# Performance work log

Hardware: AMD Instinct MI355X
Metric: run time of the kernel (lower is better)

## Reference

```python
import jax, jax.numpy as jnp
import numpy as np

N, CIN, PL, H, W, ETA, EXP = 8, 1024, 256, 64, 64, 8, 4
EPS = 1e-5

def _conv(x, w, stride=1, pad=0):
    return jax.lax.conv_general_dilated(
        x, w, (stride, stride), [(pad, pad), (pad, pad)],
        dimension_numbers=('NCHW', 'OIHW', 'NCHW'))

def _bn(x, p):
    # p: [4, C] = gamma, beta, running_mean, running_var (eval-mode BN)
    g, b, m, v = p[0], p[1], p[2], p[3]
    scale = (g / jnp.sqrt(v + EPS))[None, :, None, None]
    return (x - m[None, :, None, None]) * scale + b[None, :, None, None]

def _bn_params(key, c):
    k1, k2, k3, k4 = jax.random.split(key, 4)
    return jnp.stack([
        1.0 + 0.1 * jax.random.normal(k1, (c,)),
        0.1 * jax.random.normal(k2, (c,)),
        0.1 * jax.random.normal(k3, (c,)),
        jax.random.uniform(k4, (c,), minval=0.5, maxval=1.5)]).astype(jnp.float32)

def setup_inputs() -> dict:
    key = jax.random.key(0)
    ks = jax.random.split(key, 12)
    return {
        'x': jax.random.normal(ks[0], (N, CIN, H, W), jnp.float32),
        'norm_1': jnp.zeros((1, N + 1), jnp.float32),
        'norm_2': jnp.zeros((1, N + 1), jnp.float32),
        'flops': jnp.zeros((1, N + 1), jnp.float32),
        'ws_conv': 0.02 * jax.random.normal(ks[1], (1, CIN, 3, 3), jnp.float32),
        'ws_bias': jnp.zeros((1,), jnp.float32),
        'wc1': 0.02 * jax.random.normal(ks[2], (PL, CIN), jnp.float32),
        'bc1': jnp.zeros((PL,), jnp.float32),
        'wc2': 0.02 * jax.random.normal(ks[3], (PL, PL), jnp.float32),
        'bc2': jnp.zeros((PL,), jnp.float32),
        'w1': 0.05 * jax.random.normal(ks[4], (PL, CIN, 1, 1), jnp.float32),
        'bn1': _bn_params(ks[5], PL),
        'w2': 0.02 * jax.random.normal(ks[6], (PL, PL, 3, 3), jnp.float32),
        'bn2': _bn_params(ks[7], PL),
        'w3': 0.05 * jax.random.normal(ks[8], (PL * EXP, PL, 1, 1), jnp.float32),
        'bn3': _bn_params(ks[9], PL * EXP),
    }

def reference(x, norm_1, norm_2, flops, ws_conv, ws_bias, wc1, bc1, wc2, bc2,
              w1, bn1, w2, bn2, w3, bn3):
    n, c, h1, w1s = x.shape
    dt = x.dtype
    # ---- Mask_s: avg-pool by eta -> 3x3 conv to 1 ch -> hard gate (eval) ----
    pooled = x.reshape(n, c, h1 // ETA, ETA, w1s // ETA, ETA).mean((3, 5))
    logit_s = _conv(pooled, ws_conv, pad=1) + ws_bias[None, :, None, None]
    mask_s_m = (logit_s >= 0).astype(dt)            # [n,1,h/eta,w/eta]
    norm_s = mask_s_m.sum((1, 2, 3))                # [n]
    # ---- Mask_c1: GAP -> FC -> hard gate -> [n,PL,1,1] ----
    vec1 = x.mean((2, 3))                            # [n,CIN]
    mc1 = ((vec1 @ wc1.T + bc1) >= 0).astype(dt)[:, :, None, None]
    norm_c1 = mc1.sum((1, 2, 3))
    norm_c1_t = jnp.array([PL], dt)
    # ---- main path ----
    out = jax.nn.relu(_bn(_conv(x, w1), bn1))
    # nearest upsample of spatial mask back to (h1, w1)
    mask_s1 = jnp.repeat(jnp.repeat(mask_s_m, ETA, axis=2), ETA, axis=3)
    out = out * mc1 * mask_s1                        # eval-mode: both masks applied
    # ---- Mask_c2 on gated features ----
    vec2 = out.mean((2, 3))
    mc2 = ((vec2 @ wc2.T + bc2) >= 0).astype(dt)[:, :, None, None]
    norm_c2 = mc2.sum((1, 2, 3))
    norm_c2_t = jnp.array([PL], dt)
    out = jax.nn.relu(_bn(_conv(out, w2, pad=1), bn2))
    h2, w2s = out.shape[2], out.shape[3]
    mask_s2 = mask_s1                                # stride=1 -> same spatial size
    out = out * mc2 * mask_s2
    out = _bn(_conv(out, w3), bn3) * mask_s2
    out = jax.nn.relu(out + x)                       # identity (downsample=None)
    # ---- bookkeeping ----
    numel_s = jnp.array([mask_s_m[0].size], dt)      # 1 * h/eta * w/eta
    norm_1 = jnp.concatenate([norm_1, jnp.concatenate([norm_s, numel_s])[None]], 0)
    norm_2 = jnp.concatenate([norm_2, jnp.concatenate([norm_c1, norm_c1_t])[None]], 0)
    norm_2 = jnp.concatenate([norm_2, jnp.concatenate([norm_c2, norm_c2_t])[None]], 0)
    s_sum = mask_s2.sum((1, 2, 3))
    s_sum_1 = mask_s1.sum((1, 2, 3))
    fl = (s_sum_1 * norm_c1 * CIN
          + 9.0 * s_sum * norm_c2 * norm_c1
          + s_sum * (PL * EXP) * norm_c2)
    fl_full = jnp.array([h1 * w1s * PL * CIN
                         + 9 * h2 * w2s * PL * PL
                         + h2 * w2s * PL * PL * EXP], dt)
    flops = jnp.concatenate([flops, jnp.concatenate([fl, fl_full])[None]], 0)
    return out, norm_1, norm_2, flops
```

## Files before the change

kernel.cpp:

```cpp
#include <hip/hip_runtime.h>
#include <cstddef>
#include <cstdint>

#define NN   8
#define CIN  1024
#define PL   256
#define PE   1024
#define HW   4096
#define EPS_ 1e-5f

typedef _Float16 half8 __attribute__((ext_vector_type(8)));
typedef float floatx4 __attribute__((ext_vector_type(4)));

union HU { uint4 u4; half8 h8; };

__device__ inline uint32_t pack2(float v) {
  union { _Float16 f[2]; uint32_t u; } z;
  _Float16 h = (_Float16)v;
  z.f[0] = h;
  z.f[1] = (_Float16)(v - (float)h);
  return z.u;
}

static const size_t OFF1 = 33554432;
static const size_t OFF2 = OFF1 + 18;
static const size_t OFF3 = OFF2 + 27;

__global__ __launch_bounds__(256) void k_prep(
    const float* __restrict__ bn1, const float* __restrict__ bn2,
    const float* __restrict__ bn3, const float* __restrict__ w1,
    const float* __restrict__ w2, const float* __restrict__ w3,
    _Float16* __restrict__ w1h, _Float16* __restrict__ w1l,
    _Float16* __restrict__ w2h, _Float16* __restrict__ w2l,
    _Float16* __restrict__ w3h, _Float16* __restrict__ w3l,
    float* __restrict__ s1, float* __restrict__ t1,
    float* __restrict__ s2, float* __restrict__ t2,
    float* __restrict__ s3, float* __restrict__ t3,
    float* __restrict__ vec2) {
  int idx = blockIdx.x * 256 + threadIdx.x;
  if (idx < 262144) {
    float v = w1[idx]; _Float16 h = (_Float16)v;
    w1h[idx] = h; w1l[idx] = (_Float16)(v - (float)h);
  } else if (idx < 524288) {
    int i = idx - 262144;
    float v = w3[i]; _Float16 h = (_Float16)v;
    w3h[i] = h; w3l[i] = (_Float16)(v - (float)h);
  } else if (idx < 1114112) {
    int i = idx - 524288;
    int tap = i >> 16, rem = i & 65535, p = rem >> 8, c = rem & 255;
    float v = w2[((p << 8) + c) * 9 + tap];
    _Float16 h = (_Float16)v;
    w2h[i] = h; w2l[i] = (_Float16)(v - (float)h);
  } else if (idx < 1116160) {
    vec2[idx - 1114112] = 0.f;
  } else if (idx < 1117696) {
    int i = idx - 1116160;
    if (i < 256) {
      float g = bn1[i], b = bn1[256 + i], m = bn1[512 + i], v = bn1[768 + i];
      float s = g / sqrtf(v + EPS_);
      s1[i] = s; t1[i] = b - m * s;
    } else if (i < 512) {
      int c = i - 256;
      float g = bn2[c], b = bn2[256 + c], m = bn2[512 + c], v = bn2[768 + c];
      float s = g / sqrtf(v + EPS_);
      s2[c] = s; t2[c] = b - m * s;
    } else {
      int c = i - 512;
      float g = bn3[c], b = bn3[1024 + c], m = bn3[2048 + c], v = bn3[3072 + c];
      float s = g / sqrtf(v + EPS_);
      s3[c] = s; t3[c] = b - m * s;
    }
  }
}

__global__ __launch_bounds__(64) void k_pool(const float* __restrict__ x,
                                             float* __restrict__ pooled,
                                             float* __restrict__ vec1) {
  const int bx = blockIdx.x;
  const int n = bx >> 10, c = bx & 1023;
  const int t = threadIdx.x;
  const float* xp = x + (size_t)(n * CIN + c) * HW;
  const int g = t >> 3;
  float v1 = 0.f;
  for (int ph = 0; ph < 8; ++ph) {
    float a = 0.f;
#pragma unroll
    for (int r = 0; r < 8; ++r) a += xp[(ph * 8 + r) * 64 + t];
    a += __shfl_xor(a, 1, 64);
    a += __shfl_xor(a, 2, 64);
    a += __shfl_xor(a, 4, 64);
    if ((t & 7) == 0)
      pooled[(size_t)(n * 64 + ph * 8 + g) * 1024 + c] = a * (1.f / 64.f);
    v1 += a;
  }
  v1 += __shfl_xor(v1, 8, 64);
  v1 += __shfl_xor(v1, 16, 64);
  v1 += __shfl_xor(v1, 32, 64);
  if (t == 0) vec1[n * 1024 + c] = v1 * (1.f / 4096.f);
}

__global__ __launch_bounds__(256) void k_masks(const float* __restrict__ wsconv,
                                               const float* __restrict__ wsbias,
                                               const float* __restrict__ pooled,
                                               float* __restrict__ masks) {
  const int bid = blockIdx.x;
  const int n = bid >> 6, cell = bid & 63, ph = cell >> 3, pw = cell & 7;
  const int tid = threadIdx.x;
  const float* pl = pooled + (size_t)n * 64 * 1024;
  float acc = 0.f;
#pragma unroll
  for (int kh = 0; kh < 3; ++kh) {
    int py = ph + kh - 1;
    if (py < 0 || py > 7) continue;
#pragma unroll
    for (int kw = 0; kw < 3; ++kw) {
      int px = pw + kw - 1;
      if (px < 0 || px > 7) continue;
      float4 pv = *(const float4*)(pl + (size_t)(py * 8 + px) * 1024 + tid * 4);
      int k = kh * 3 + kw;
      acc += pv.x * wsconv[(tid * 4 + 0) * 9 + k] + pv.y * wsconv[(tid * 4 + 1) * 9 + k]
           + pv.z * wsconv[(tid * 4 + 2) * 9 + k] + pv.w * wsconv[(tid * 4 + 3) * 9 + k];
    }
  }
  __shared__ float red[256];
  red[tid] = acc;
  __syncthreads();
  for (int s = 128; s > 0; s >>= 1) {
    if (tid < s) red[tid] += red[tid + s];
    __syncthreads();
  }
  if (tid == 0) masks[n * 64 + cell] = (red[0] + wsbias[0] >= 0.f) ? 1.f : 0.f;
}

__global__ __launch_bounds__(64) void k_mc1(const float* __restrict__ wc1,
                                            const float* __restrict__ bc1,
                                            const float* __restrict__ vec1,
                                            float* __restrict__ mc1) {
  const int bx = blockIdx.x;
  const int n = bx >> 8, p = bx & 255;
  const int t = threadIdx.x;
  const float* v = vec1 + n * 1024;
  const float* wr = wc1 + (size_t)p * 1024;
  float acc = 0.f;
#pragma unroll
  for (int j = 0; j < 16; ++j) acc += v[t + 64 * j] * wr[t + 64 * j];
  for (int m = 1; m < 64; m <<= 1) acc += __shfl_xor(acc, m, 64);
  if (t == 0) mc1[n * 256 + p] = (acc + bc1[p] >= 0.f) ? 1.f : 0.f;
}

__global__ __launch_bounds__(256) void k_xsplit(const float* __restrict__ x,
                                                _Float16* __restrict__ xh,
                                                _Float16* __restrict__ xl) {
  const int hw0 = blockIdx.x * 64, c0 = blockIdx.y * 64, n = blockIdx.z;
  const int t = threadIdx.x;
  __shared__ float Tt[64][65];
#pragma unroll
  for (int j = 0; j < 4; ++j) {
    int rc = (t >> 4) + j * 16;
    int col = (t & 15) * 4;
    float4 v = *(const float4*)(x + ((size_t)(n * 1024) + c0 + rc) * 4096 + hw0 + col);
    Tt[col + 0][rc] = v.x; Tt[col + 1][rc] = v.y;
    Tt[col + 2][rc] = v.z; Tt[col + 3][rc] = v.w;
  }
  __syncthreads();
  const int hwl = t >> 2, part = t & 3;
  size_t ob = ((size_t)(n * 4096) + hw0 + hwl) * 1024 + c0 + part * 16;
#pragma unroll
  for (int k2 = 0; k2 < 2; ++k2) {
    half8 vh, vl;
#pragma unroll
    for (int e = 0; e < 8; ++e) {
      float v = Tt[hwl][part * 16 + k2 * 8 + e];
      _Float16 hh = (_Float16)v;
      vh[e] = hh; vl[e] = (_Float16)(v - (float)hh);
    }
    *(half8*)(xh + ob + k2 * 8) = vh;
    *(half8*)(xl + ob + k2 * 8) = vl;
  }
}

__global__ __launch_bounds__(256) void k_gemm1(
    const _Float16* __restrict__ xh, const _Float16* __restrict__ xl,
    const _Float16* __restrict__ w1h, const _Float16* __restrict__ w1l,
    const float* __restrict__ s1, const float* __restrict__ t1,
    const float* __restrict__ mc1, const float* __restrict__ masks,
    _Float16* __restrict__ o1h, _Float16* __restrict__ o1l) {
  const int hw0 = blockIdx.x * 128, p0 = blockIdx.y * 128, n = blockIdx.z;
  const int t = threadIdx.x;
  const int lane = t & 63, w = t >> 6;
  const int l15 = lane & 15, l4 = lane >> 4;
  const int wr = w >> 1, wc = w & 1;
  __shared__ __align__(16) char smem[40960];
  _Float16* LB = (_Float16*)smem;
  floatx4 acc[4][4] = {};
  const size_t nb = (size_t)(n * 4096) + hw0;
  for (int ks = 0; ks < 32; ++ks) {
    const int c0 = ks * 32;
    half8 tmp[8];
#pragma unroll
    for (int j = 0; j < 8; ++j) {
      int u = t + 256 * j;
      int kind = u >> 9, rem = u & 511, row = rem >> 2, q = rem & 3;
      const _Float16* src;
      if (kind == 0)      src = w1h + (size_t)(p0 + row) * 1024 + c0 + q * 8;
      else if (kind == 1) src = w1l + (size_t)(p0 + row) * 1024 + c0 + q * 8;
      else if (kind == 2) src = xh + (nb + row) * 1024 + c0 + q * 8;
      else                src = xl + (nb + row) * 1024 + c0 + q * 8;
      tmp[j] = *(const half8*)src;
    }
    __syncthreads();
#pragma unroll
    for (int j = 0; j < 8; ++j) {
      int u = t + 256 * j;
      int kind = u >> 9, rem = u & 511, row = rem >> 2, q = rem & 3;
      *(half8*)(LB + kind * 5120 + row * 40 + q * 8) = tmp[j];
    }
    __syncthreads();
    half8 ah[4], al[4], bh[4], bl[4];
#pragma unroll
    for (int i = 0; i < 4; ++i) {
      int r = (wr * 64 + i * 16 + l15) * 40 + l4 * 8;
      ah[i] = *(const half8*)(LB + r);
      al[i] = *(const half8*)(LB + 5120 + r);
    }
#pragma unroll
    for (int j = 0; j < 4; ++j) {
      int r = (wc * 64 + j * 16 + l15) * 40 + l4 * 8;
      bh[j] = *(const half8*)(LB + 10240 + r);
      bl[j] = *(const half8*)(LB + 15360 + r);
    }
#pragma unroll
    for (int i = 0; i < 4; ++i)
#pragma unroll
      for (int j = 0; j < 4; ++j) {
        acc[i][j] = __builtin_amdgcn_mfma_f32_16x16x32_f16(ah[i], bh[j], acc[i][j], 0, 0, 0);
        acc[i][j] = __builtin_amdgcn_mfma_f32_16x16x32_f16(ah[i], bl[j], acc[i][j], 0, 0, 0);
        acc[i][j] = __builtin_amdgcn_mfma_f32_16x16x32_f16(al[i], bh[j], acc[i][j], 0, 0, 0);
      }
  }
  uint32_t (*T)[132] = (uint32_t(*)[132])smem;
  const int n64 = n * 64;
  const float* mc1n = mc1 + n * 256;
  for (int h = 0; h < 2; ++h) {
    __syncthreads();
    if (wc == h) {
#pragma unroll
      for (int j = 0; j < 4; ++j) {
        int nl = j * 16 + l15;
        int pix = hw0 + h * 64 + nl;
        float msk = masks[n64 + ((pix >> 9) << 3) + ((pix & 63) >> 3)];
#pragma unroll
        for (int i = 0; i < 4; ++i) {
          uint32_t pk[4];
#pragma unroll
          for (int r = 0; r < 4; ++r) {
            int m = wr * 64 + i * 16 + l4 * 4 + r;
            int p = p0 + m;
            float val = fmaxf(fmaf(acc[i][j][r], s1[p], t1[p]), 0.f) * (mc1n[p] * msk);
            pk[r] = pack2(val);
          }
          *(uint4*)&T[nl][wr * 64 + i * 16 + l4 * 4] = *(uint4*)pk;
        }
      }
    }
    __syncthreads();
    {
      int row = t >> 2, seg = t & 3;
      int pix = hw0 + h * 64 + row;
      _Float16* dh = o1h + ((size_t)(n * 4096) + pix) * 256 + p0 + seg * 32;
      _Float16* dl = o1l + ((size_t)(n * 4096) + pix) * 256 + p0 + seg * 32;
#pragma unroll
      for (int k2 = 0; k2 < 4; ++k2) {
        uint4 a = *(uint4*)&T[row][seg * 32 + k2 * 8];
        uint4 b = *(uint4*)&T[row][seg * 32 + k2 * 8 + 4];
        uint4 hv = make_uint4((a.x & 0xFFFFu) | (a.y << 16), (a.z & 0xFFFFu) | (a.w << 16),
                              (b.x & 0xFFFFu) | (b.y << 16), (b.z & 0xFFFFu) | (b.w << 16));
        uint4 lv = make_uint4((a.x >> 16) | (a.y & 0xFFFF0000u), (a.z >> 16) | (a.w & 0xFFFF0000u),
                              (b.x >> 16) | (b.y & 0xFFFF0000u), (b.z >> 16) | (b.w & 0xFFFF0000u));
        *(uint4*)(dh + k2 * 8) = hv;
        *(uint4*)(dl + k2 * 8) = lv;
      }
    }
  }
}

__global__ __launch_bounds__(256) void k_vec2(const _Float16* __restrict__ o1h,
                                              const _Float16* __restrict__ o1l,
                                              float* __restrict__ vec2) {
  const int n = blockIdx.x >> 5, ch = blockIdx.x & 31;
  const int t = threadIdx.x;
  const _Float16* bh = o1h + ((size_t)(n * 4096) + ch * 128) * 256 + t;
  const _Float16* bl = o1l + ((size_t)(n * 4096) + ch * 128) * 256 + t;
  float s = 0.f;
  for (int i = 0; i < 128; ++i)
    s += (float)bh[(size_t)i * 256] + (float)bl[(size_t)i * 256];
  atomicAdd(&vec2[n * 256 + t], s * (1.f / 4096.f));
}

__global__ __launch_bounds__(64) void k_mc2(const float* __restrict__ wc2,
                                            const float* __restrict__ bc2,
                                            const float* __restrict__ vec2,
                                            float* __restrict__ mc2) {
  const int bx = blockIdx.x;
  const int n = bx >> 8, p = bx & 255;
  const int t = threadIdx.x;
  const float* v = vec2 + n * 256;
  const float* wr = wc2 + (size_t)p * 256;
  float acc = 0.f;
#pragma unroll
  for (int j = 0; j < 4; ++j) acc += v[t + 64 * j] * wr[t + 64 * j];
  for (int m = 1; m < 64; m <<= 1) acc += __shfl_xor(acc, m, 64);
  if (t == 0) mc2[n * 256 + p] = (acc + bc2[p] >= 0.f) ? 1.f : 0.f;
}

__global__ __launch_bounds__(256) void k_gemm2(
    const _Float16* __restrict__ o1h, const _Float16* __restrict__ o1l,
    const _Float16* __restrict__ w2h, const _Float16* __restrict__ w2l,
    const float* __restrict__ s2, const float* __restrict__ t2,
    const float* __restrict__ mc2, const float* __restrict__ masks,
    _Float16* __restrict__ o2h, _Float16* __restrict__ o2l) {
  const int bt = blockIdx.x, p0 = blockIdx.y * 128, n = blockIdx.z;
  const int hw0 = bt * 128;
  const int t = threadIdx.x;
  const int lane = t & 63, w = t >> 6;
  const int l15 = lane & 15, l4 = lane >> 4;
  const int wr = w >> 1, wc = w & 1;
  __shared__ __align__(16) char smem[62720];
  _Float16* LB = (_Float16*)smem;
  floatx4 acc[4][4] = {};
  const size_t onb = (size_t)(n * 4096);
  const int row0 = bt * 2 - 1;
  for (int c0 = 0; c0 < 256; c0 += 32) {
    HU st[9];
#pragma unroll
    for (int j2 = 0; j2 < 9; ++j2) {
      int u = t + 256 * j2;
      st[j2].u4 = make_uint4(0u, 0u, 0u, 0u);
      if (u < 2112) {
        int kind = (u >= 1056) ? 1 : 0;
        int rem = u - kind * 1056;
        int pix = rem >> 2, q = rem & 3;
        int sr = pix / 66, sc = pix - sr * 66;
        int gr = row0 + sr, gc = sc - 1;
        if (gr >= 0 && gr < 64 && gc >= 0 && gc < 64) {
          const _Float16* src = (kind ? o1l : o1h) + (onb + gr * 64 + gc) * 256 + c0 + q * 8;
          st[j2].h8 = *(const half8*)src;
        }
      }
    }
    __syncthreads();
#pragma unroll
    for (int j2 = 0; j2 < 9; ++j2) {
      int u = t + 256 * j2;
      if (u < 2112) {
        int kind = (u >= 1056) ? 1 : 0;
        int rem = u - kind * 1056;
        int pix = rem >> 2, q = rem & 3;
        *(half8*)(LB + kind * 10560 + pix * 40 + q * 8) = st[j2].h8;
      }
    }
    for (int tap = 0; tap < 9; ++tap) {
      const int kh = tap / 3, kw = tap - kh * 3;
      HU at[4];
#pragma unroll
      for (int j2 = 0; j2 < 4; ++j2) {
        int u = t + 256 * j2;
        int kind = u >> 9, rem = u & 511, row = rem >> 2, q = rem & 3;
        const _Float16* src = (kind ? w2l : w2h) + (size_t)tap * 65536 +
                              (size_t)(p0 + row) * 256 + c0 + q * 8;
        at[j2].h8 = *(const half8*)src;
      }
      __syncthreads();
#pragma unroll
      for (int j2 = 0; j2 < 4; ++j2) {
        int u = t + 256 * j2;
        int kind = u >> 9, rem = u & 511, row = rem >> 2, q = rem & 3;
        *(half8*)(LB + 21120 + kind * 5120 + row * 40 + q * 8) = at[j2].h8;
      }
      __syncthreads();
      half8 ah[4], al[4], bh[4], bl[4];
#pragma unroll
      for (int i = 0; i < 4; ++i) {
        int r = (wr * 64 + i * 16 + l15) * 40 + l4 * 8;
        ah[i] = *(const half8*)(LB + 21120 + r);
        al[i] = *(const half8*)(LB + 26240 + r);
      }
#pragma unroll
      for (int j = 0; j < 4; ++j) {
        int nl = wc * 64 + j * 16 + l15;
        int pi = ((nl >> 6) + kh) * 66 + (nl & 63) + kw;
        bh[j] = *(const half8*)(LB + pi * 40 + l4 * 8);
        bl[j] = *(const half8*)(LB + 10560 + pi * 40 + l4 * 8);
      }
#pragma unroll
      for (int i = 0; i < 4; ++i)
#pragma unroll
        for (int j = 0; j < 4; ++j) {
          acc[i][j] = __builtin_amdgcn_mfma_f32_16x16x32_f16(ah[i], bh[j], acc[i][j], 0, 0, 0);
          acc[i][j] = __builtin_amdgcn_mfma_f32_16x16x32_f16(ah[i], bl[j], acc[i][j], 0, 0, 0);
          acc[i][j] = __builtin_amdgcn_mfma_f32_16x16x32_f16(al[i], bh[j], acc[i][j], 0, 0, 0);
        }
    }
    __syncthreads();
  }
  uint32_t (*T)[132] = (uint32_t(*)[132])smem;
  const int n64 = n * 64;
  const float* mc2n = mc2 + n * 256;
  for (int h = 0; h < 2; ++h) {
    __syncthreads();
    if (wc == h) {
#pragma unroll
      for (int j = 0; j < 4; ++j) {
        int nl = j * 16 + l15;
        int pix = hw0 + h * 64 + nl;
        float msk = masks[n64 + ((pix >> 9) << 3) + ((pix & 63) >> 3)];
#pragma unroll
        for (int i = 0; i < 4; ++i) {
          uint32_t pk[4];
#pragma unroll
          for (int r = 0; r < 4; ++r) {
            int m = wr * 64 + i * 16 + l4 * 4 + r;
            int p = p0 + m;
            float val = fmaxf(fmaf(acc[i][j][r], s2[p], t2[p]), 0.f) * (mc2n[p] * msk);
            pk[r] = pack2(val);
          }
          *(uint4*)&T[nl][wr * 64 + i * 16 + l4 * 4] = *(uint4*)pk;
        }
      }
    }
    __syncthreads();
    {
      int row = t >> 2, seg = t & 3;
      int pix = hw0 + h * 64 + row;
      _Float16* dh = o2h + ((size_t)(n * 4096) + pix) * 256 + p0 + seg * 32;
      _Float16* dl = o2l + ((size_t)(n * 4096) + pix) * 256 + p0 + seg * 32;
#pragma unroll
      for (int k2 = 0; k2 < 4; ++k2) {
        uint4 a = *(uint4*)&T[row][seg * 32 + k2 * 8];
        uint4 b = *(uint4*)&T[row][seg * 32 + k2 * 8 + 4];
        uint4 hv = make_uint4((a.x & 0xFFFFu) | (a.y << 16), (a.z & 0xFFFFu) | (a.w << 16),
                              (b.x & 0xFFFFu) | (b.y << 16), (b.z & 0xFFFFu) | (b.w << 16));
        uint4 lv = make_uint4((a.x >> 16) | (a.y & 0xFFFF0000u), (a.z >> 16) | (a.w & 0xFFFF0000u),
                              (b.x >> 16) | (b.y & 0xFFFF0000u), (b.z >> 16) | (b.w & 0xFFFF0000u));
        *(uint4*)(dh + k2 * 8) = hv;
        *(uint4*)(dl + k2 * 8) = lv;
      }
    }
  }
}

__global__ __launch_bounds__(256) void k_gemm3(
    const _Float16* __restrict__ o2h, const _Float16* __restrict__ o2l,
    const _Float16* __restrict__ w3h, const _Float16* __restrict__ w3l,
    const float* __restrict__ s3, const float* __restrict__ t3,
    const float* __restrict__ masks, const float* __restrict__ x,
    float* __restrict__ out) {
  const int hw0 = blockIdx.x * 128, p0 = blockIdx.y * 128, n = blockIdx.z;
  const int t = threadIdx.x;
  const int lane = t & 63, w = t >> 6;
  const int l15 = lane & 15, l4 = lane >> 4;
  const int wr = w >> 1, wc = w & 1;
  __shared__ __align__(16) char smem[40960];
  _Float16* LB = (_Float16*)smem;
  floatx4 acc[4][4] = {};
  const size_t nb = (size_t)(n * 4096) + hw0;
  for (int ks = 0; ks < 8; ++ks) {
    const int c0 = ks * 32;
    half8 tmp[8];
#pragma unroll
    for (int j = 0; j < 8; ++j) {
      int u = t + 256 * j;
      int kind = u >> 9, rem = u & 511, row = rem >> 2, q = rem & 3;
      const _Float16* src;
      if (kind == 0)      src = w3h + (size_t)(p0 + row) * 256 + c0 + q * 8;
      else if (kind == 1) src = w3l + (size_t)(p0 + row) * 256 + c0 + q * 8;
      else if (kind == 2) src = o2h + (nb + row) * 256 + c0 + q * 8;
      else                src = o2l + (nb + row) * 256 + c0 + q * 8;
      tmp[j] = *(const half8*)src;
    }
    __syncthreads();
#pragma unroll
    for (int j = 0; j < 8; ++j) {
      int u = t + 256 * j;
      int kind = u >> 9, rem = u & 511, row = rem >> 2, q = rem & 3;
      *(half8*)(LB + kind * 5120 + row * 40 + q * 8) = tmp[j];
    }
    __syncthreads();
    half8 ah[4], al[4], bh[4], bl[4];
#pragma unroll
    for (int i = 0; i < 4; ++i) {
      int r = (wr * 64 + i * 16 + l15) * 40 + l4 * 8;
      ah[i] = *(const half8*)(LB + r);
      al[i] = *(const half8*)(LB + 5120 + r);
    }
#pragma unroll
    for (int j = 0; j < 4; ++j) {
      int r = (wc * 64 + j * 16 + l15) * 40 + l4 * 8;
      bh[j] = *(const half8*)(LB + 10240 + r);
      bl[j] = *(const half8*)(LB + 15360 + r);
    }
#pragma unroll
    for (int i = 0; i < 4; ++i)
#pragma unroll
      for (int j = 0; j < 4; ++j) {
        acc[i][j] = __builtin_amdgcn_mfma_f32_16x16x32_f16(ah[i], bh[j], acc[i][j], 0, 0, 0);
        acc[i][j] = __builtin_amdgcn_mfma_f32_16x16x32_f16(ah[i], bl[j], acc[i][j], 0, 0, 0);
        acc[i][j] = __builtin_amdgcn_mfma_f32_16x16x32_f16(al[i], bh[j], acc[i][j], 0, 0, 0);
      }
  }
  const int n64 = n * 64;
  float msk[4];
#pragma unroll
  for (int j = 0; j < 4; ++j) {
    int pix = hw0 + wc * 64 + j * 16 + l15;
    msk[j] = masks[n64 + ((pix >> 9) << 3) + ((pix & 63) >> 3)];
  }
#pragma unroll
  for (int i = 0; i < 4; ++i)
#pragma unroll
    for (int r = 0; r < 4; ++r) {
      int m = wr * 64 + i * 16 + l4 * 4 + r;
      int pe = p0 + m;
      float sc = s3[pe], sh = t3[pe];
      size_t rowoff = ((size_t)(n * 1024) + pe) * 4096 + hw0;
#pragma unroll
      for (int j = 0; j < 4; ++j) {
        int nl = wc * 64 + j * 16 + l15;
        float val = fmaf(acc[i][j][r], sc, sh) * msk[j];
        size_t off = rowoff + nl;
        out[off] = fmaxf(val + x[off], 0.f);
      }
    }
}

__global__ __launch_bounds__(64) void k_book(const float* __restrict__ n1in,
                                             const float* __restrict__ n2in,
                                             const float* __restrict__ flin,
                                             const float* __restrict__ masks,
                                             const float* __restrict__ mc1,
                                             const float* __restrict__ mc2,
                                             float* __restrict__ out) {
  const int t = threadIdx.x;
  if (t < 9) {
    out[OFF1 + t] = n1in[t];
    out[OFF2 + t] = n2in[t];
    out[OFF3 + t] = flin[t];
  }
  if (t < 8) {
    float ns = 0.f, nc1 = 0.f, nc2 = 0.f;
    for (int i = 0; i < 64; ++i) ns += masks[t * 64 + i];
    for (int i = 0; i < 256; ++i) nc1 += mc1[t * 256 + i];
    for (int i = 0; i < 256; ++i) nc2 += mc2[t * 256 + i];
    out[OFF1 + 9 + t] = ns;
    out[OFF2 + 9 + t] = nc1;
    out[OFF2 + 18 + t] = nc2;
    const float s = ns * 64.f;
    const float term1 = (s * nc1) * 1024.f;
    const float term2 = ((9.f * s) * nc2) * nc1;
    const float term3 = (s * 1024.f) * nc2;
    out[OFF3 + 9 + t] = (term1 + term2) + term3;
  }
  if (t == 9) {
    out[OFF1 + 17] = 64.f;
    out[OFF2 + 17] = 256.f;
    out[OFF2 + 26] = 256.f;
    out[OFF3 + 17] = 4563402752.f;
  }
}

extern "C" void kernel_launch(void* const* d_in, const int* in_sizes, int n_in,
                              void* d_out, int out_size, void* d_ws, size_t ws_size,
                              hipStream_t stream) {
  (void)in_sizes; (void)n_in; (void)out_size; (void)ws_size;
  const float* x      = (const float*)d_in[0];
  const float* n1in   = (const float*)d_in[1];
  const float* n2in   = (const float*)d_in[2];
  const float* flin   = (const float*)d_in[3];
  const float* wsconv = (const float*)d_in[4];
  const float* wsbias = (const float*)d_in[5];
  const float* wc1    = (const float*)d_in[6];
  const float* bc1    = (const float*)d_in[7];
  const float* wc2    = (const float*)d_in[8];
  const float* bc2    = (const float*)d_in[9];
  const float* w1     = (const float*)d_in[10];
  const float* bn1    = (const float*)d_in[11];
  const float* w2     = (const float*)d_in[12];
  const float* bn2    = (const float*)d_in[13];
  const float* w3     = (const float*)d_in[14];
  const float* bn3    = (const float*)d_in[15];
  float* out = (float*)d_out;

  _Float16* xh = (_Float16*)d_out;
  _Float16* xl = xh + 33554432;

  char* W = (char*)d_ws;
  _Float16* o1h = (_Float16*)(W);
  _Float16* o1l = (_Float16*)(W + 16777216);
  _Float16* o2h = (_Float16*)(W + 33554432);
  _Float16* o2l = (_Float16*)(W + 50331648);
  _Float16* w1h = (_Float16*)(W + 67108864);
  _Float16* w1l = (_Float16*)(W + 67633152);
  _Float16* w2h = (_Float16*)(W + 68157440);
  _Float16* w2l = (_Float16*)(W + 69337088);
  _Float16* w3h = (_Float16*)(W + 70516736);
  _Float16* w3l = (_Float16*)(W + 71041024);
  float* pooled = (float*)(W + 71565312);
  float* vec1   = (float*)(W + 73662464);
  float* vec2   = (float*)(W + 73695232);
  float* masksP = (float*)(W + 73703424);
  float* mc1    = (float*)(W + 73705472);
  float* mc2    = (float*)(W + 73713664);
  float* s1     = (float*)(W + 73721856);
  float* t1     = (float*)(W + 73722880);
  float* s2     = (float*)(W + 73723904);
  float* t2     = (float*)(W + 73724928);
  float* s3     = (float*)(W + 73725952);
  float* t3     = (float*)(W + 73730048);

  hipLaunchKernelGGL(k_prep, dim3(4366), dim3(256), 0, stream,
                     bn1, bn2, bn3, w1, w2, w3, w1h, w1l, w2h, w2l, w3h, w3l,
                     s1, t1, s2, t2, s3, t3, vec2);
  hipLaunchKernelGGL(k_pool, dim3(NN * CIN), dim3(64), 0, stream, x, pooled, vec1);
  hipLaunchKernelGGL(k_masks, dim3(NN * 64), dim3(256), 0, stream, wsconv, wsbias, pooled, masksP);
  hipLaunchKernelGGL(k_mc1, dim3(NN * PL), dim3(64), 0, stream, wc1, bc1, vec1, mc1);
  hipLaunchKernelGGL(k_xsplit, dim3(64, 16, NN), dim3(256), 0, stream, x, xh, xl);
  hipLaunchKernelGGL(k_gemm1, dim3(32, 2, NN), dim3(256), 0, stream,
                     xh, xl, w1h, w1l, s1, t1, mc1, masksP, o1h, o1l);
  hipLaunchKernelGGL(k_vec2, dim3(NN * 32), dim3(256), 0, stream, o1h, o1l, vec2);
  hipLaunchKernelGGL(k_mc2, dim3(NN * PL), dim3(64), 0, stream, wc2, bc2, vec2, mc2);
  hipLaunchKernelGGL(k_gemm2, dim3(32, 2, NN), dim3(256), 0, stream,
                     o1h, o1l, w2h, w2l, s2, t2, mc2, masksP, o2h, o2l);
  hipLaunchKernelGGL(k_gemm3, dim3(32, 8, NN), dim3(256), 0, stream,
                     o2h, o2l, w3h, w3l, s3, t3, masksP, x, out);
  hipLaunchKernelGGL(k_book, dim3(1), dim3(64), 0, stream,
                     n1in, n2in, flin, masksP, mc1, mc2, out);
}
```

Baseline: 685.8 us.

## Pre-swizzle weights into MFMA fragment layout and fuse pooling into x split

Weights are rearranged once in the prep kernel into a per-lane MFMA fragment layout with hi/lo halves interleaved. All three GEMMs then load the A operand straight from global memory into registers instead of staging it through LDS, which shrinks shared memory and, in gemm2, drops the per-tap barriers. The separate pooling kernel is removed: the transpose/split kernel now also accumulates pooled averages with atomics, and a small new kernel reduces them to the channel means. This saves one full read of x and some LDS traffic, at the cost of uncoalesced-looking global weight loads relying on cache, plus atomic contention and a nondeterministic summation order in pooled.

```diff
diff --git a/kernel.cpp b/kernel.cpp
--- a/kernel.cpp
+++ b/kernel.cpp
@@ -30,31 +30,40 @@
     const float* __restrict__ bn1, const float* __restrict__ bn2,
     const float* __restrict__ bn3, const float* __restrict__ w1,
     const float* __restrict__ w2, const float* __restrict__ w3,
-    _Float16* __restrict__ w1h, _Float16* __restrict__ w1l,
-    _Float16* __restrict__ w2h, _Float16* __restrict__ w2l,
-    _Float16* __restrict__ w3h, _Float16* __restrict__ w3l,
+    _Float16* __restrict__ w1f, _Float16* __restrict__ w2f,
+    _Float16* __restrict__ w3f,
     float* __restrict__ s1, float* __restrict__ t1,
     float* __restrict__ s2, float* __restrict__ t2,
     float* __restrict__ s3, float* __restrict__ t3,
-    float* __restrict__ vec2) {
-  int idx = blockIdx.x * 256 + threadIdx.x;
-  if (idx < 262144) {
+    float* __restrict__ pooled, float* __restrict__ vec2) {
+  unsigned idx = blockIdx.x * 256 + threadIdx.x;
+  if (idx < 262144u) {
+    int p = idx >> 10, c = idx & 1023;
     float v = w1[idx]; _Float16 h = (_Float16)v;
-    w1h[idx] = h; w1l[idx] = (_Float16)(v - (float)h);
-  } else if (idx < 524288) {
-    int i = idx - 262144;
+    int lane = (((c & 31) >> 3) << 4) | (p & 15);
+    size_t base = (size_t)(((c >> 5) * 16 + (p >> 4))) * 1024 + lane * 8 + (c & 7);
+    w1f[base] = h; w1f[base + 512] = (_Float16)(v - (float)h);
+  } else if (idx < 524288u) {
+    unsigned i = idx - 262144u;
+    int p = i >> 8, c = i & 255;
     float v = w3[i]; _Float16 h = (_Float16)v;
-    w3h[i] = h; w3l[i] = (_Float16)(v - (float)h);
-  } else if (idx < 1114112) {
-    int i = idx - 524288;
-    int tap = i >> 16, rem = i & 65535, p = rem >> 8, c = rem & 255;
-    float v = w2[((p << 8) + c) * 9 + tap];
-    _Float16 h = (_Float16)v;
-    w2h[i] = h; w2l[i] = (_Float16)(v - (float)h);
-  } else if (idx < 1116160) {
-    vec2[idx - 1114112] = 0.f;
-  } else if (idx < 1117696) {
-    int i = idx - 1116160;
+    int lane = (((c & 31) >> 3) << 4) | (p & 15);
+    size_t base = (size_t)((c >> 5) * 64 + (p >> 4)) * 1024 + lane * 8 + (c & 7);
+    w3f[base] = h; w3f[base + 512] = (_Float16)(v - (float)h);
+  } else if (idx < 1114112u) {
+    unsigned i = idx - 524288u;
+    unsigned p = i / 2304u, rem = i - p * 2304u;
+    unsigned c = rem / 9u, tap = rem - c * 9u;
+    float v = w2[i]; _Float16 h = (_Float16)v;
+    int lane = (((c & 31) >> 3) << 4) | (p & 15);
+    size_t base = (size_t)((tap * 8 + (c >> 5)) * 16 + (p >> 4)) * 1024 + lane * 8 + (c & 7);
+    w2f[base] = h; w2f[base + 512] = (_Float16)(v - (float)h);
+  } else if (idx < 1638400u) {
+    pooled[idx - 1114112u] = 0.f;
+  } else if (idx < 1640448u) {
+    vec2[idx - 1638400u] = 0.f;
+  } else if (idx < 1641984u) {
+    int i = idx - 1640448u;
     if (i < 256) {
       float g = bn1[i], b = bn1[256 + i], m = bn1[512 + i], v = bn1[768 + i];
       float s = g / sqrtf(v + EPS_);
@@ -73,30 +82,62 @@
   }
 }
 
-__global__ __launch_bounds__(64) void k_pool(const float* __restrict__ x,
-                                             float* __restrict__ pooled,
-                                             float* __restrict__ vec1) {
+__global__ __launch_bounds__(256) void k_xsplit(const float* __restrict__ x,
+                                                _Float16* __restrict__ xh,
+                                                _Float16* __restrict__ xl,
+                                                float* __restrict__ pooled) {
   const int bx = blockIdx.x;
-  const int n = bx >> 10, c = bx & 1023;
-  const int t = threadIdx.x;
-  const float* xp = x + (size_t)(n * CIN + c) * HW;
-  const int g = t >> 3;
-  float v1 = 0.f;
-  for (int ph = 0; ph < 8; ++ph) {
-    float a = 0.f;
-#pragma unroll
-    for (int r = 0; r < 8; ++r) a += xp[(ph * 8 + r) * 64 + t];
-    a += __shfl_xor(a, 1, 64);
-    a += __shfl_xor(a, 2, 64);
-    a += __shfl_xor(a, 4, 64);
-    if ((t & 7) == 0)
-      pooled[(size_t)(n * 64 + ph * 8 + g) * 1024 + c] = a * (1.f / 64.f);
-    v1 += a;
-  }
-  v1 += __shfl_xor(v1, 8, 64);
-  v1 += __shfl_xor(v1, 16, 64);
-  v1 += __shfl_xor(v1, 32, 64);
-  if (t == 0) vec1[n * 1024 + c] = v1 * (1.f / 4096.f);
+  const int hw0 = bx * 64, c0 = blockIdx.y * 64, n = blockIdx.z;
+  const int t = threadIdx.x;
+  __shared__ float Tt[64][65];
+#pragma unroll
+  for (int j = 0; j < 4; ++j) {
+    int rc = (t >> 4) + j * 16;
+    int col = (t & 15) * 4;
+    float4 v = *(const float4*)(x + ((size_t)(n * 1024) + c0 + rc) * 4096 + hw0 + col);
+    Tt[col + 0][rc] = v.x; Tt[col + 1][rc] = v.y;
+    Tt[col + 2][rc] = v.z; Tt[col + 3][rc] = v.w;
+  }
+  __syncthreads();
+  {
+    const int ch = t & 63, grp = t >> 6;
+    const int pr = bx >> 3;
+#pragma unroll
+    for (int cc = 0; cc < 2; ++cc) {
+      int pc = grp * 2 + cc;
+      float s = 0.f;
+#pragma unroll
+      for (int px = 0; px < 8; ++px) s += Tt[pc * 8 + px][ch];
+      atomicAdd(&pooled[(size_t)(n * 64 + pr * 8 + pc) * 1024 + c0 + ch], s * (1.f / 64.f));
+    }
+  }
+  const int hwl = t >> 2, part = t & 3;
+  size_t ob = ((size_t)(n * 4096) + hw0 + hwl) * 1024 + c0 + part * 16;
+#pragma unroll
+  for (int k2 = 0; k2 < 2; ++k2) {
+    half8 vh, vl;
+#pragma unroll
+    for (int e = 0; e < 8; ++e) {
+      float v = Tt[hwl][part * 16 + k2 * 8 + e];
+      _Float16 hh = (_Float16)v;
+      vh[e] = hh; vl[e] = (_Float16)(v - (float)hh);
+    }
+    *(half8*)(xh + ob + k2 * 8) = vh;
+    *(half8*)(xl + ob + k2 * 8) = vl;
+  }
+}
+
+__global__ __launch_bounds__(256) void k_vec1(const float* __restrict__ pooled,
+                                              float* __restrict__ vec1) {
+  const int n = blockIdx.x, t = threadIdx.x;
+#pragma unroll
+  for (int j = 0; j < 4; ++j) {
+    int c = j * 256 + t;
+    float s = 0.f;
+    for (int cell = 0; cell < 64; ++cell)
+      s += pooled[(size_t)(n * 64 + cell) * 1024 + c];
+    vec1[n * 1024 + c] = s * (1.f / 64.f);
+  }
 }
 
 __global__ __launch_bounds__(256) void k_masks(const float* __restrict__ wsconv,
@@ -148,40 +189,9 @@
   if (t == 0) mc1[n * 256 + p] = (acc + bc1[p] >= 0.f) ? 1.f : 0.f;
 }
 
-__global__ __launch_bounds__(256) void k_xsplit(const float* __restrict__ x,
-                                                _Float16* __restrict__ xh,
-                                                _Float16* __restrict__ xl) {
-  const int hw0 = blockIdx.x * 64, c0 = blockIdx.y * 64, n = blockIdx.z;
-  const int t = threadIdx.x;
-  __shared__ float Tt[64][65];
-#pragma unroll
-  for (int j = 0; j < 4; ++j) {
-    int rc = (t >> 4) + j * 16;
-    int col = (t & 15) * 4;
-    float4 v = *(const float4*)(x + ((size_t)(n * 1024) + c0 + rc) * 4096 + hw0 + col);
-    Tt[col + 0][rc] = v.x; Tt[col + 1][rc] = v.y;
-    Tt[col + 2][rc] = v.z; Tt[col + 3][rc] = v.w;
-  }
-  __syncthreads();
-  const int hwl = t >> 2, part = t & 3;
-  size_t ob = ((size_t)(n * 4096) + hw0 + hwl) * 1024 + c0 + part * 16;
-#pragma unroll
-  for (int k2 = 0; k2 < 2; ++k2) {
-    half8 vh, vl;
-#pragma unroll
-    for (int e = 0; e < 8; ++e) {
-      float v = Tt[hwl][part * 16 + k2 * 8 + e];
-      _Float16 hh = (_Float16)v;
-      vh[e] = hh; vl[e] = (_Float16)(v - (float)hh);
-    }
-    *(half8*)(xh + ob + k2 * 8) = vh;
-    *(half8*)(xl + ob + k2 * 8) = vl;
-  }
-}
-
 __global__ __launch_bounds__(256) void k_gemm1(
     const _Float16* __restrict__ xh, const _Float16* __restrict__ xl,
-    const _Float16* __restrict__ w1h, const _Float16* __restrict__ w1l,
+    const _Float16* __restrict__ w1f,
     const float* __restrict__ s1, const float* __restrict__ t1,
     const float* __restrict__ mc1, const float* __restrict__ masks,
     _Float16* __restrict__ o1h, _Float16* __restrict__ o1l) {
@@ -190,44 +200,42 @@
   const int lane = t & 63, w = t >> 6;
   const int l15 = lane & 15, l4 = lane >> 4;
   const int wr = w >> 1, wc = w & 1;
-  __shared__ __align__(16) char smem[40960];
+  __shared__ __align__(16) char smem[33792];
   _Float16* LB = (_Float16*)smem;
   floatx4 acc[4][4] = {};
   const size_t nb = (size_t)(n * 4096) + hw0;
-  for (int ks = 0; ks < 32; ++ks) {
-    const int c0 = ks * 32;
-    half8 tmp[8];
-#pragma unroll
-    for (int j = 0; j < 8; ++j) {
+  const _Float16* wfp = w1f + (size_t)((p0 >> 4) + wr * 4) * 1024 + lane * 8;
+  for (int kc = 0; kc < 32; ++kc) {
+    const int c0 = kc * 32;
+    half8 tmp[4];
+#pragma unroll
+    for (int j = 0; j < 4; ++j) {
       int u = t + 256 * j;
       int kind = u >> 9, rem = u & 511, row = rem >> 2, q = rem & 3;
-      const _Float16* src;
-      if (kind == 0)      src = w1h + (size_t)(p0 + row) * 1024 + c0 + q * 8;
-      else if (kind == 1) src = w1l + (size_t)(p0 + row) * 1024 + c0 + q * 8;
-      else if (kind == 2) src = xh + (nb + row) * 1024 + c0 + q * 8;
-      else                src = xl + (nb + row) * 1024 + c0 + q * 8;
+      const _Float16* src = (kind ? xl : xh) + (nb + row) * 1024 + c0 + q * 8;
       tmp[j] = *(const half8*)src;
     }
-    __syncthreads();
-#pragma unroll
-    for (int j = 0; j < 8; ++j) {
+    half8 ah[4], al[4];
+#pragma unroll
+    for (int i = 0; i < 4; ++i) {
+      const _Float16* ap = wfp + (size_t)(kc * 16 + i) * 1024;
+      ah[i] = *(const half8*)ap;
+      al[i] = *(const half8*)(ap + 512);
+    }
+    __syncthreads();
+#pragma unroll
+    for (int j = 0; j < 4; ++j) {
       int u = t + 256 * j;
       int kind = u >> 9, rem = u & 511, row = rem >> 2, q = rem & 3;
       *(half8*)(LB + kind * 5120 + row * 40 + q * 8) = tmp[j];
     }
     __syncthreads();
-    half8 ah[4], al[4], bh[4], bl[4];
-#pragma unroll
-    for (int i = 0; i < 4; ++i) {
-      int r = (wr * 64 + i * 16 + l15) * 40 + l4 * 8;
-      ah[i] = *(const half8*)(LB + r);
-      al[i] = *(const half8*)(LB + 5120 + r);
-    }
+    half8 bh[4], bl[4];
 #pragma unroll
     for (int j = 0; j < 4; ++j) {
       int r = (wc * 64 + j * 16 + l15) * 40 + l4 * 8;
-      bh[j] = *(const half8*)(LB + 10240 + r);
-      bl[j] = *(const half8*)(LB + 15360 + r);
+      bh[j] = *(const half8*)(LB + r);
+      bl[j] = *(const half8*)(LB + 5120 + r);
     }
 #pragma unroll
     for (int i = 0; i < 4; ++i)
@@ -315,7 +323,7 @@
 
 __global__ __launch_bounds__(256) void k_gemm2(
     const _Float16* __restrict__ o1h, const _Float16* __restrict__ o1l,
-    const _Float16* __restrict__ w2h, const _Float16* __restrict__ w2l,
+    const _Float16* __restrict__ w2f,
     const float* __restrict__ s2, const float* __restrict__ t2,
     const float* __restrict__ mc2, const float* __restrict__ masks,
     _Float16* __restrict__ o2h, _Float16* __restrict__ o2l) {
@@ -325,12 +333,14 @@
   const int lane = t & 63, w = t >> 6;
   const int l15 = lane & 15, l4 = lane >> 4;
   const int wr = w >> 1, wc = w & 1;
-  __shared__ __align__(16) char smem[62720];
+  __shared__ __align__(16) char smem[42240];
   _Float16* LB = (_Float16*)smem;
   floatx4 acc[4][4] = {};
   const size_t onb = (size_t)(n * 4096);
   const int row0 = bt * 2 - 1;
-  for (int c0 = 0; c0 < 256; c0 += 32) {
+  const _Float16* wfp = w2f + (size_t)((p0 >> 4) + wr * 4) * 1024 + lane * 8;
+  for (int kc = 0; kc < 8; ++kc) {
+    const int c0 = kc * 32;
     HU st[9];
 #pragma unroll
     for (int j2 = 0; j2 < 9; ++j2) {
@@ -359,36 +369,20 @@
         *(half8*)(LB + kind * 10560 + pix * 40 + q * 8) = st[j2].h8;
       }
     }
+    __syncthreads();
+#pragma unroll 1
     for (int tap = 0; tap < 9; ++tap) {
       const int kh = tap / 3, kw = tap - kh * 3;
-      HU at[4];
-#pragma unroll
-      for (int j2 = 0; j2 < 4; ++j2) {
-        int u = t + 256 * j2;
-        int kind = u >> 9, rem = u & 511, row = rem >> 2, q = rem & 3;
-        const _Float16* src = (kind ? w2l : w2h) + (size_t)tap * 65536 +
-                              (size_t)(p0 + row) * 256 + c0 + q * 8;
-        at[j2].h8 = *(const half8*)src;
-      }
-      __syncthreads();
-#pragma unroll
-      for (int j2 = 0; j2 < 4; ++j2) {
-        int u = t + 256 * j2;
-        int kind = u >> 9, rem = u & 511, row = rem >> 2, q = rem & 3;
-        *(half8*)(LB + 21120 + kind * 5120 + row * 40 + q * 8) = at[j2].h8;
-      }
-      __syncthreads();
       half8 ah[4], al[4], bh[4], bl[4];
 #pragma unroll
       for (int i = 0; i < 4; ++i) {
-        int r = (wr * 64 + i * 16 + l15) * 40 + l4 * 8;
-        ah[i] = *(const half8*)(LB + 21120 + r);
-        al[i] = *(const half8*)(LB + 26240 + r);
+        const _Float16* ap = wfp + (size_t)(((tap * 8 + kc) * 16) + i) * 1024;
+        ah[i] = *(const half8*)ap;
+        al[i] = *(const half8*)(ap + 512);
       }
 #pragma unroll
       for (int j = 0; j < 4; ++j) {
-        int nl = wc * 64 + j * 16 + l15;
-        int pi = ((nl >> 6) + kh) * 66 + (nl & 63) + kw;
+        int pi = (wc + kh) * 66 + j * 16 + l15 + kw;
         bh[j] = *(const half8*)(LB + pi * 40 + l4 * 8);
         bl[j] = *(const half8*)(LB + 10560 + pi * 40 + l4 * 8);
       }
@@ -401,7 +395,6 @@
           acc[i][j] = __builtin_amdgcn_mfma_f32_16x16x32_f16(al[i], bh[j], acc[i][j], 0, 0, 0);
         }
     }
-    __syncthreads();
   }
   uint32_t (*T)[132] = (uint32_t(*)[132])smem;
   const int n64 = n * 64;
@@ -451,7 +444,7 @@
 
 __global__ __launch_bounds__(256) void k_gemm3(
     const _Float16* __restrict__ o2h, const _Float16* __restrict__ o2l,
-    const _Float16* __restrict__ w3h, const _Float16* __restrict__ w3l,
+    const _Float16* __restrict__ w3f,
     const float* __restrict__ s3, const float* __restrict__ t3,
     const float* __restrict__ masks, const float* __restrict__ x,
     float* __restrict__ out) {
@@ -460,44 +453,42 @@
   const int lane = t & 63, w = t >> 6;
   const int l15 = lane & 15, l4 = lane >> 4;
   const int wr = w >> 1, wc = w & 1;
-  __shared__ __align__(16) char smem[40960];
+  __shared__ __align__(16) char smem[20480];
   _Float16* LB = (_Float16*)smem;
   floatx4 acc[4][4] = {};
   const size_t nb = (size_t)(n * 4096) + hw0;
-  for (int ks = 0; ks < 8; ++ks) {
-    const int c0 = ks * 32;
-    half8 tmp[8];
-#pragma unroll
-    for (int j = 0; j < 8; ++j) {
+  const _Float16* wfp = w3f + (size_t)((p0 >> 4) + wr * 4) * 1024 + lane * 8;
+  for (int kc = 0; kc < 8; ++kc) {
+    const int c0 = kc * 32;
+    half8 tmp[4];
+#pragma unroll
+    for (int j = 0; j < 4; ++j) {
       int u = t + 256 * j;
       int kind = u >> 9, rem = u & 511, row = rem >> 2, q = rem & 3;
-      const _Float16* src;
-      if (kind == 0)      src = w3h + (size_t)(p0 + row) * 256 + c0 + q * 8;
-      else if (kind == 1) src = w3l + (size_t)(p0 + row) * 256 + c0 + q * 8;
-      else if (kind == 2) src = o2h + (nb + row) * 256 + c0 + q * 8;
-      else                src = o2l + (nb + row) * 256 + c0 + q * 8;
+      const _Float16* src = (kind ? o2l : o2h) + (nb + row) * 256 + c0 + q * 8;
       tmp[j] = *(const half8*)src;
     }
-    __syncthreads();
-#pragma unroll
-    for (int j = 0; j < 8; ++j) {
+    half8 ah[4], al[4];
+#pragma unroll
+    for (int i = 0; i < 4; ++i) {
+      const _Float16* ap = wfp + (size_t)(kc * 64 + i) * 1024;
+      ah[i] = *(const half8*)ap;
+      al[i] = *(const half8*)(ap + 512);
+    }
+    __syncthreads();
+#pragma unroll
+    for (int j = 0; j < 4; ++j) {
       int u = t + 256 * j;
       int kind = u >> 9, rem = u & 511, row = rem >> 2, q = rem & 3;
       *(half8*)(LB + kind * 5120 + row * 40 + q * 8) = tmp[j];
     }
     __syncthreads();
-    half8 ah[4], al[4], bh[4], bl[4];
-#pragma unroll
-    for (int i = 0; i < 4; ++i) {
-      int r = (wr * 64 + i * 16 + l15) * 40 + l4 * 8;
-      ah[i] = *(const half8*)(LB + r);
-      al[i] = *(const half8*)(LB + 5120 + r);
-    }
+    half8 bh[4], bl[4];
 #pragma unroll
     for (int j = 0; j < 4; ++j) {
       int r = (wc * 64 + j * 16 + l15) * 40 + l4 * 8;
-      bh[j] = *(const half8*)(LB + 10240 + r);
-      bl[j] = *(const half8*)(LB + 15360 + r);
+      bh[j] = *(const half8*)(LB + r);
+      bl[j] = *(const half8*)(LB + 5120 + r);
     }
 #pragma unroll
     for (int i = 0; i < 4; ++i)
@@ -507,6 +498,7 @@
         acc[i][j] = __builtin_amdgcn_mfma_f32_16x16x32_f16(ah[i], bl[j], acc[i][j], 0, 0, 0);
         acc[i][j] = __builtin_amdgcn_mfma_f32_16x16x32_f16(al[i], bh[j], acc[i][j], 0, 0, 0);
       }
+    __syncthreads();
   }
   const int n64 = n * 64;
   float msk[4];
@@ -598,12 +590,9 @@
   _Float16* o1l = (_Float16*)(W + 16777216);
   _Float16* o2h = (_Float16*)(W + 33554432);
   _Float16* o2l = (_Float16*)(W + 50331648);
-  _Float16* w1h = (_Float16*)(W + 67108864);
-  _Float16* w1l = (_Float16*)(W + 67633152);
-  _Float16* w2h = (_Float16*)(W + 68157440);
-  _Float16* w2l = (_Float16*)(W + 69337088);
-  _Float16* w3h = (_Float16*)(W + 70516736);
-  _Float16* w3l = (_Float16*)(W + 71041024);
+  _Float16* w1f = (_Float16*)(W + 67108864);
+  _Float16* w2f = (_Float16*)(W + 68157440);
+  _Float16* w3f = (_Float16*)(W + 70516736);
   float* pooled = (float*)(W + 71565312);
   float* vec1   = (float*)(W + 73662464);
   float* vec2   = (float*)(W + 73695232);
@@ -617,21 +606,21 @@
   float* s3     = (float*)(W + 73725952);
   float* t3     = (float*)(W + 73730048);
 
-  hipLaunchKernelGGL(k_prep, dim3(4366), dim3(256), 0, stream,
-                     bn1, bn2, bn3, w1, w2, w3, w1h, w1l, w2h, w2l, w3h, w3l,
-                     s1, t1, s2, t2, s3, t3, vec2);
-  hipLaunchKernelGGL(k_pool, dim3(NN * CIN), dim3(64), 0, stream, x, pooled, vec1);
+  hipLaunchKernelGGL(k_prep, dim3(6414), dim3(256), 0, stream,
+                     bn1, bn2, bn3, w1, w2, w3, w1f, w2f, w3f,
+                     s1, t1, s2, t2, s3, t3, pooled, vec2);
+  hipLaunchKernelGGL(k_xsplit, dim3(64, 16, NN), dim3(256), 0, stream, x, xh, xl, pooled);
+  hipLaunchKernelGGL(k_vec1, dim3(NN), dim3(256), 0, stream, pooled, vec1);
   hipLaunchKernelGGL(k_masks, dim3(NN * 64), dim3(256), 0, stream, wsconv, wsbias, pooled, masksP);
   hipLaunchKernelGGL(k_mc1, dim3(NN * PL), dim3(64), 0, stream, wc1, bc1, vec1, mc1);
-  hipLaunchKernelGGL(k_xsplit, dim3(64, 16, NN), dim3(256), 0, stream, x, xh, xl);
   hipLaunchKernelGGL(k_gemm1, dim3(32, 2, NN), dim3(256), 0, stream,
-                     xh, xl, w1h, w1l, s1, t1, mc1, masksP, o1h, o1l);
+                     xh, xl, w1f, s1, t1, mc1, masksP, o1h, o1l);
   hipLaunchKernelGGL(k_vec2, dim3(NN * 32), dim3(256), 0, stream, o1h, o1l, vec2);
   hipLaunchKernelGGL(k_mc2, dim3(NN * PL), dim3(64), 0, stream, wc2, bc2, vec2, mc2);
   hipLaunchKernelGGL(k_gemm2, dim3(32, 2, NN), dim3(256), 0, stream,
-                     o1h, o1l, w2h, w2l, s2, t2, mc2, masksP, o2h, o2l);
+                     o1h, o1l, w2f, s2, t2, mc2, masksP, o2h, o2l);
   hipLaunchKernelGGL(k_gemm3, dim3(32, 8, NN), dim3(256), 0, stream,
-                     o2h, o2l, w3h, w3l, s3, t3, masksP, x, out);
+                     o2h, o2l, w3f, s3, t3, masksP, x, out);
   hipLaunchKernelGGL(k_book, dim3(1), dim3(64), 0, stream,
                      n1in, n2in, flin, masksP, mc1, mc2, out);
 }
```

Result: slower. 747.3 us (+9.0%).
